# Performance work log

Hardware: AMD Instinct MI355X
Metric: run time of the kernel (lower is better)

The kernel has to match this reference:

```python
import jax, jax.numpy as jnp
import numpy as np

N = 131072        # total packed tokens
D = 256           # input_dim
E = 512           # embed_dim
B = 16            # number of batches (len(cu_seqlens)-1)
NLAYERS = 64      # max distinct layer ids per batch


def setup_inputs() -> dict:
    key = jax.random.key(0)
    ks = jax.random.split(key, 8)
    feats = jax.random.normal(ks[0], (N, D), dtype=jnp.float32)
    cu_seqlens = jnp.arange(0, N + 1, N // B, dtype=jnp.int32)  # [B+1]
    layer_ids = jax.random.randint(ks[1], (N,), 0, NLAYERS, dtype=jnp.int32)
    # Linear params stored as [in, out] (y = x @ W + b), matching torch Linear math.
    Wa = jax.random.normal(ks[2], (D, 1), jnp.float32) * 0.05
    ba = jnp.zeros((1,), jnp.float32)
    W1 = jax.random.normal(ks[3], (3 * D, E), jnp.float32) * 0.02
    b1 = jnp.zeros((E,), jnp.float32)
    W2 = jax.random.normal(ks[4], (E, D), jnp.float32) * 0.02
    b2 = jnp.zeros((D,), jnp.float32)
    Wc = jax.random.normal(ks[5], (2 * D, D), jnp.float32) * 0.02
    bc = jnp.zeros((D,), jnp.float32)
    return dict(feats=feats, cu_seqlens=cu_seqlens, layer_ids=layer_ids,
                Wa=Wa, ba=ba, W1=W1, b1=b1, W2=W2, b2=b2, Wc=Wc, bc=bc)


def _forward(feats, cu_seqlens, layer_ids, Wa, ba, W1, b1, W2, b2, Wc, bc):
    n = feats.shape[0]
    nseg = B * NLAYERS
    # batch id of each token from the cumulative sequence lengths
    batch_ids = jnp.searchsorted(cu_seqlens, jnp.arange(n, dtype=jnp.int32), side='right') - 1
    # global (batch, layer) segment id -> vectorizes the per-batch scatter loop
    seg = batch_ids * NLAYERS + layer_ids

    counts = jax.ops.segment_sum(jnp.ones((n,), feats.dtype), seg, num_segments=nseg)  # [nseg]
    sums = jax.ops.segment_sum(feats, seg, num_segments=nseg)                           # [nseg, D]
    avg_pool = sums / jnp.maximum(counts, 1.0)[:, None]
    max_pool = jax.ops.segment_max(feats, seg, num_segments=nseg)
    max_pool = jnp.where(counts[:, None] > 0, max_pool, 0.0)  # empty segments -> 0 (never gathered)

    # attention softmax over all tokens of each batch (dim=0 within the batch slice)
    logits = (feats @ Wa + ba)[:, 0]                                    # [n]
    m = jax.ops.segment_max(logits, batch_ids, num_segments=B)          # [B]
    e = jnp.exp(logits - m[batch_ids])
    z = jax.ops.segment_sum(e, batch_ids, num_segments=B)               # [B]
    w = e / z[batch_ids]                                                # [n]
    attention_pool = jax.ops.segment_sum(feats * w[:, None], seg, num_segments=nseg)

    pooled = jnp.concatenate([avg_pool, max_pool, attention_pool], axis=1)  # [nseg, 3D]
    h = jax.nn.gelu(pooled @ W1 + b1, approximate=False)
    layer_feats = h @ W2 + b2                                               # [nseg, D]

    gathered = layer_feats[seg]                                             # [n, D]
    out = jnp.concatenate([gathered, feats], axis=1) @ Wc + bc              # [n, D]
    return out


def reference(feats, cu_seqlens, layer_ids, Wa, ba, W1, b1, W2, b2, Wc, bc):
    return _forward(feats, cu_seqlens, layer_ids, Wa, ba, W1, b1, W2, b2, Wc, bc)
```

## Files before the change

kernel.cpp:

```cpp
#include <hip/hip_runtime.h>
#include <hip/hip_bf16.h>
#include <math.h>

#define NTOK 131072
#define DIM  256
#define EDIM 512
#define NB   16
#define NL   64
#define NSEG (NB*NL)
#define K3D  768
#define K2D  512
#define HB   64
#define K4CH 256

typedef __attribute__((ext_vector_type(8))) short short8;
typedef __attribute__((ext_vector_type(4))) float f32x4;

static __device__ __forceinline__ unsigned fcode(float x){
  unsigned b = __float_as_uint(x);
  return (b & 0x80000000u) ? ~b : (b | 0x80000000u);
}
static __device__ __forceinline__ float fdecode(unsigned c){
  unsigned b = (c & 0x80000000u) ? (c ^ 0x80000000u) : ~c;
  return __uint_as_float(b);
}
#define NEG_INF_CODE 0x007FFFFFu

static __device__ __forceinline__ short f2bf(float x){
  union { __hip_bfloat16 h; short s; } u; u.h = __float2bfloat16(x); return u.s;
}
static __device__ __forceinline__ float bf2f(short s){
  union { float f; unsigned u; } u; u.u = ((unsigned)(unsigned short)s) << 16; return u.f;
}

__global__ __launch_bounds__(256) void k0_transpose(const float* __restrict__ W1, const float* __restrict__ W2,
                                                    const float* __restrict__ Wc,
                                                    short* __restrict__ W1t, short* __restrict__ W2t,
                                                    short* __restrict__ Wct, unsigned* __restrict__ bmax){
  if (blockIdx.x == 0 && threadIdx.x < NB) bmax[threadIdx.x] = NEG_INF_CODE;
  __shared__ short tile[64][65];
  int b = blockIdx.x;
  const float* src; short* dst; int K, N, kt, nt;
  if (b < 96){ src=W1; dst=W1t; K=768; N=512; kt=b/8;  nt=b%8;  }
  else if (b < 128){ int c=b-96;  src=W2; dst=W2t; K=512; N=256; kt=c/4; nt=c%4; }
  else             { int c=b-128; src=Wc; dst=Wct; K=512; N=256; kt=c/4; nt=c%4; }
  int k0 = kt*64, n0 = nt*64;
  for (int e = threadIdx.x; e < 4096; e += 256){
    int r = e >> 6, c = e & 63;
    tile[c][r] = f2bf(src[(size_t)(k0+r)*N + n0 + c]);
  }
  __syncthreads();
  for (int e = threadIdx.x; e < 4096; e += 256){
    int r = e >> 6, c = e & 63;
    dst[(size_t)(n0+r)*K + k0 + c] = tile[r][c];
  }
}

template<int WRITEB>
__global__ __launch_bounds__(256) void k1_logits(const float* __restrict__ feats, const int* __restrict__ cu,
    const int* __restrict__ layer_ids, const float* __restrict__ Wa, const float* __restrict__ ba,
    float* __restrict__ logits, int* __restrict__ seg, unsigned* __restrict__ bmax,
    short* __restrict__ featsb){
  __shared__ int      lcu[NB];
  __shared__ unsigned lbm[NB];
  int tid = threadIdx.x;
  if (tid < NB){ lcu[tid] = cu[tid+1]; lbm[tid] = NEG_INF_CODE; }
  int s = tid & 15;
  int rowoff = tid >> 4;
  float4 w0 = *(const float4*)(Wa + s*4);
  float4 w1 = *(const float4*)(Wa + 64 + s*4);
  float4 w2 = *(const float4*)(Wa + 128 + s*4);
  float4 w3 = *(const float4*)(Wa + 192 + s*4);
  float bav = ba[0];
  __syncthreads();
#pragma unroll
  for (int it = 0; it < 4; ++it){
    int r = (blockIdx.x + it*2048)*16 + rowoff;
    const float4* fp = (const float4*)(feats + (size_t)r*DIM);
    float4 x0 = fp[s], x1 = fp[16+s], x2 = fp[32+s], x3 = fp[48+s];
    float a = x0.x*w0.x + x0.y*w0.y + x0.z*w0.z + x0.w*w0.w
            + x1.x*w1.x + x1.y*w1.y + x1.z*w1.z + x1.w*w1.w
            + x2.x*w2.x + x2.y*w2.y + x2.z*w2.z + x2.w*w2.w
            + x3.x*w3.x + x3.y*w3.y + x3.z*w3.z + x3.w*w3.w;
    if (WRITEB){
      short4* ob = (short4*)(featsb + (size_t)r*DIM);
      short4 v;
      v.x=f2bf(x0.x); v.y=f2bf(x0.y); v.z=f2bf(x0.z); v.w=f2bf(x0.w); ob[s]    = v;
      v.x=f2bf(x1.x); v.y=f2bf(x1.y); v.z=f2bf(x1.z); v.w=f2bf(x1.w); ob[16+s] = v;
      v.x=f2bf(x2.x); v.y=f2bf(x2.y); v.z=f2bf(x2.z); v.w=f2bf(x2.w); ob[32+s] = v;
      v.x=f2bf(x3.x); v.y=f2bf(x3.y); v.z=f2bf(x3.z); v.w=f2bf(x3.w); ob[48+s] = v;
    }
    a += __shfl_xor(a, 1);
    a += __shfl_xor(a, 2);
    a += __shfl_xor(a, 4);
    a += __shfl_xor(a, 8);
    if (s == 0){
      float lg = a + bav;
      logits[r] = lg;
      int b = 0;
#pragma unroll
      for (int j = 0; j < NB-1; ++j) b += (lcu[j] <= r) ? 1 : 0;
      seg[r] = b*NL + layer_ids[r];
      atomicMax(&lbm[b], fcode(lg));
    }
  }
  __syncthreads();
  if (tid < NB && lbm[tid] != NEG_INF_CODE) atomicMax(&bmax[tid], lbm[tid]);
}

__global__ __launch_bounds__(256) void k2_softmax_z(const float* __restrict__ logits, const int* __restrict__ cu,
    const unsigned* __restrict__ bmax, float* __restrict__ bz){
  __shared__ float red[256];
  int b = blockIdx.x;
  int s = cu[b], e = cu[b+1];
  float m = fdecode(bmax[b]);
  float acc = 0.f;
  for (int i = s + threadIdx.x; i < e; i += 256)
    acc += expf(logits[i] - m);
  red[threadIdx.x] = acc; __syncthreads();
  for (int off = 128; off; off >>= 1){
    if (threadIdx.x < off) red[threadIdx.x] += red[threadIdx.x + off];
    __syncthreads();
  }
  if (threadIdx.x == 0) bz[b] = red[0];
}

__global__ __launch_bounds__(256) void k3a_hist(const int* __restrict__ seg, int* __restrict__ hist){
  __shared__ int h[NSEG];
  for (int i = threadIdx.x; i < NSEG; i += 256) h[i] = 0;
  __syncthreads();
  int base = blockIdx.x * (NTOK/HB);
  for (int i = threadIdx.x; i < NTOK/HB; i += 256) atomicAdd(&h[seg[base+i]], 1);
  __syncthreads();
  for (int i = threadIdx.x; i < NSEG; i += 256) hist[(size_t)blockIdx.x*NSEG + i] = h[i];
}

__global__ __launch_bounds__(1024) void k3b_scan(int* __restrict__ hist, int* __restrict__ segstart){
  __shared__ int sc[NSEG];
  int s = threadIdx.x;
  int tot = 0;
#pragma unroll
  for (int b = 0; b < HB; ++b) tot += hist[(size_t)b*NSEG + s];
  sc[s] = tot; __syncthreads();
  for (int off = 1; off < NSEG; off <<= 1){
    int v = (s >= off) ? sc[s-off] : 0;
    __syncthreads();
    sc[s] += v;
    __syncthreads();
  }
  int segbase = sc[s] - tot;
  segstart[s] = segbase;
  if (s == 0) segstart[NSEG] = NTOK;
  int run = segbase;
#pragma unroll
  for (int b = 0; b < HB; ++b){
    int c = hist[(size_t)b*NSEG + s];
    hist[(size_t)b*NSEG + s] = run;
    run += c;
  }
}

__global__ __launch_bounds__(256) void k3c_scatter(const int* __restrict__ seg, const int* __restrict__ hist,
                                                   int* __restrict__ sorted){
  __shared__ int cur[NSEG];
  for (int i = threadIdx.x; i < NSEG; i += 256) cur[i] = hist[(size_t)blockIdx.x*NSEG + i];
  __syncthreads();
  int base = blockIdx.x * (NTOK/HB);
  for (int i = threadIdx.x; i < NTOK/HB; i += 256){
    int sg = seg[base+i];
    int p = atomicAdd(&cur[sg], 1);
    sorted[p] = base+i;
  }
}

template<int USEB>
__global__ __launch_bounds__(256) void k4_pool(const float* __restrict__ feats, const short* __restrict__ featsb,
    const int* __restrict__ sorted, const int* __restrict__ segstart,
    const float* __restrict__ logits, const unsigned* __restrict__ bmax, const float* __restrict__ bz,
    short* __restrict__ pooledb){
  __shared__ float redS[4][DIM];
  __shared__ float redM[4][DIM];
  __shared__ float redA[4][DIM];
  __shared__ int   ltok[K4CH];
  __shared__ float lwgt[K4CH];
  int sgi = blockIdx.x;
  int b = sgi >> 6;
  int s = segstart[sgi], e = segstart[sgi+1];
  int cnt = e - s;
  float m = fdecode(bmax[b]);
  float invz = 1.0f / bz[b];
  int lane = threadIdx.x & 63, grp = threadIdx.x >> 6;
  float4 sum = make_float4(0.f,0.f,0.f,0.f), att = make_float4(0.f,0.f,0.f,0.f);
  float4 mx  = make_float4(-INFINITY,-INFINITY,-INFINITY,-INFINITY);
  for (int c0 = s; c0 < e; c0 += K4CH){
    int csz = min(K4CH, e - c0);
    for (int j = threadIdx.x; j < csz; j += 256){
      int t = sorted[c0 + j];
      ltok[j] = t;
      lwgt[j] = expf(logits[t] - m) * invz;
    }
    __syncthreads();
    for (int j = grp; j < csz; j += 4){
      int tok = ltok[j];
      float w = lwgt[j];
      float4 x;
      if (USEB){
        short4 h = *(const short4*)(featsb + (size_t)tok*DIM + lane*4);
        x = make_float4(bf2f(h.x), bf2f(h.y), bf2f(h.z), bf2f(h.w));
      } else {
        x = *(const float4*)(feats + (size_t)tok*DIM + lane*4);
      }
      sum.x += x.x; sum.y += x.y; sum.z += x.z; sum.w += x.w;
      mx.x = fmaxf(mx.x, x.x); mx.y = fmaxf(mx.y, x.y);
      mx.z = fmaxf(mx.z, x.z); mx.w = fmaxf(mx.w, x.w);
      att.x += x.x*w; att.y += x.y*w; att.z += x.z*w; att.w += x.w*w;
    }
    __syncthreads();
  }
  *(float4*)&redS[grp][lane*4] = sum;
  *(float4*)&redM[grp][lane*4] = mx;
  *(float4*)&redA[grp][lane*4] = att;
  __syncthreads();
  int d = threadIdx.x;
  float rs = redS[0][d] + redS[1][d] + redS[2][d] + redS[3][d];
  float rm = fmaxf(fmaxf(redM[0][d], redM[1][d]), fmaxf(redM[2][d], redM[3][d]));
  float ra = redA[0][d] + redA[1][d] + redA[2][d] + redA[3][d];
  float inv = 1.0f / (float)(cnt > 1 ? cnt : 1);
  size_t rb_ = (size_t)sgi * K3D;
  pooledb[rb_ + d]         = f2bf(rs * inv);
  pooledb[rb_ + DIM + d]   = f2bf(cnt > 0 ? rm : 0.f);
  pooledb[rb_ + 2*DIM + d] = f2bf(ra);
}

template<int GELU>
__global__ __launch_bounds__(256) void gemm64(const short* __restrict__ A, const short* __restrict__ Bt,
    const float* __restrict__ bias, short* __restrict__ Cout, int K, int ldc){
  __shared__ short lA[64][40];
  __shared__ short lB[64][40];
  int tid = threadIdx.x;
  int wave = tid >> 6, lane = tid & 63;
  int wm = wave >> 1, wn = wave & 1;
  int rb = blockIdx.x * 64, cb = blockIdx.y * 64;
  int l15 = lane & 15, lg = lane >> 4;
  f32x4 acc[2][2] = {};
  int srow = tid >> 2, skg = tid & 3;
  for (int ks = 0; ks < K; ks += 32){
    __syncthreads();
    *(short8*)&lA[srow][skg*8] = *(const short8*)(A  + (size_t)(rb+srow)*K + ks + skg*8);
    *(short8*)&lB[srow][skg*8] = *(const short8*)(Bt + (size_t)(cb+srow)*K + ks + skg*8);
    __syncthreads();
    short8 af[2], bf[2];
#pragma unroll
    for (int f = 0; f < 2; ++f){
      af[f] = *(const short8*)&lA[wm*32 + f*16 + l15][lg*8];
      bf[f] = *(const short8*)&lB[wn*32 + f*16 + l15][lg*8];
    }
#pragma unroll
    for (int fm = 0; fm < 2; ++fm)
#pragma unroll
      for (int fn = 0; fn < 2; ++fn)
        acc[fm][fn] = __builtin_amdgcn_mfma_f32_16x16x32_bf16(af[fm], bf[fn], acc[fm][fn], 0, 0, 0);
  }
#pragma unroll
  for (int fm = 0; fm < 2; ++fm)
#pragma unroll
    for (int fn = 0; fn < 2; ++fn){
      int col = cb + wn*32 + fn*16 + l15;
      float bcv = bias[col];
#pragma unroll
      for (int r = 0; r < 4; ++r){
        int row = rb + wm*32 + fm*16 + lg*4 + r;
        float v = acc[fm][fn][r] + bcv;
        if (GELU) v = 0.5f * v * (1.0f + erff(v * 0.70710678118f));
        Cout[(size_t)row*ldc + col] = f2bf(v);
      }
    }
}

template<int USEB>
__global__ __launch_bounds__(1024, 4) void k5_final(const float* __restrict__ feats,
    const short* __restrict__ featsb, const short* __restrict__ lfb,
    const int* __restrict__ seg, const short* __restrict__ Wct, const float* __restrict__ bc,
    float* __restrict__ out){
  __shared__ short lA[2][128][72];
  __shared__ short lB[2][256][72];
  int tid = threadIdx.x;
  int wave = tid >> 6, lane = tid & 63;
  int wm = wave >> 2, wn = wave & 3;
  int bid = (int)blockIdx.x;
  int swz = (bid & 7) * 128 + (bid >> 3);
  int rb = swz * 128;
  int l15 = lane & 15, lg = lane >> 4;
  int arow = tid >> 3, akg = tid & 7;
  int brow0 = tid >> 3, brow1 = (tid + 1024) >> 3, bkg = tid & 7;
  const short* lfbp = lfb + (size_t)seg[rb + arow]*DIM + akg*8;
  const short* fbp  = featsb + (size_t)(rb + arow)*DIM + akg*8;
  const float* ffp  = feats  + (size_t)(rb + arow)*DIM + akg*8;
  const short* wp0 = Wct + (size_t)brow0*K2D + bkg*8;
  const short* wp1 = Wct + (size_t)brow1*K2D + bkg*8;
  short8 ra, rb0, rb1; float4 fa0, fa1;
  auto LOAD = [&](int t){
    if (t < 4)      ra = *(const short8*)(lfbp + t*64);
    else if (USEB)  ra = *(const short8*)(fbp + (t-4)*64);
    else { const float* p = ffp + (size_t)(t-4)*64; fa0 = *(const float4*)p; fa1 = *(const float4*)(p+4); }
    rb0 = *(const short8*)(wp0 + t*64);
    rb1 = *(const short8*)(wp1 + t*64);
  };
  auto WRITE = [&](int t){
    int buf = t & 1;
    if (!USEB && t >= 4){
      short8 v;
      v[0]=f2bf(fa0.x); v[1]=f2bf(fa0.y); v[2]=f2bf(fa0.z); v[3]=f2bf(fa0.w);
      v[4]=f2bf(fa1.x); v[5]=f2bf(fa1.y); v[6]=f2bf(fa1.z); v[7]=f2bf(fa1.w);
      *(short8*)&lA[buf][arow][akg*8] = v;
    } else {
      *(short8*)&lA[buf][arow][akg*8] = ra;
    }
    *(short8*)&lB[buf][brow0][bkg*8] = rb0;
    *(short8*)&lB[buf][brow1][bkg*8] = rb1;
  };
  f32x4 acc[2][4] = {};
  LOAD(0); WRITE(0); LOAD(1);
  __syncthreads();
  for (int ks = 0; ks < 8; ++ks){
    int cur = ks & 1;
    if (ks < 7) WRITE(ks+1);
    if (ks < 6) LOAD(ks+2);
#pragma unroll
    for (int kk = 0; kk < 2; ++kk){
      short8 af[2], bf[4];
#pragma unroll
      for (int f = 0; f < 2; ++f)
        af[f] = *(const short8*)&lA[cur][wm*32 + f*16 + l15][kk*32 + lg*8];
#pragma unroll
      for (int f = 0; f < 4; ++f)
        bf[f] = *(const short8*)&lB[cur][wn*64 + f*16 + l15][kk*32 + lg*8];
#pragma unroll
      for (int fm = 0; fm < 2; ++fm)
#pragma unroll
        for (int fn = 0; fn < 4; ++fn)
          acc[fm][fn] = __builtin_amdgcn_mfma_f32_16x16x32_bf16(af[fm], bf[fn], acc[fm][fn], 0, 0, 0);
    }
    __syncthreads();
  }
#pragma unroll
  for (int fm = 0; fm < 2; ++fm)
#pragma unroll
    for (int fn = 0; fn < 4; ++fn){
      int col = wn*64 + fn*16 + l15;
      float bcv = bc[col];
#pragma unroll
      for (int r = 0; r < 4; ++r){
        int row = rb + wm*32 + fm*16 + lg*4 + r;
        out[(size_t)row*DIM + col] = acc[fm][fn][r] + bcv;
      }
    }
}

extern "C" void kernel_launch(void* const* d_in, const int* in_sizes, int n_in,
                              void* d_out, int out_size, void* d_ws, size_t ws_size,
                              hipStream_t stream){
  const float* feats     = (const float*)d_in[0];
  const int*   cu        = (const int*)d_in[1];
  const int*   layer_ids = (const int*)d_in[2];
  const float* Wa        = (const float*)d_in[3];
  const float* ba        = (const float*)d_in[4];
  const float* W1        = (const float*)d_in[5];
  const float* b1        = (const float*)d_in[6];
  const float* W2        = (const float*)d_in[7];
  const float* b2        = (const float*)d_in[8];
  const float* Wc        = (const float*)d_in[9];
  const float* bc        = (const float*)d_in[10];
  float* out = (float*)d_out;

  char* w = (char*)d_ws;
  auto alloc = [&](size_t bytes)->char*{ char* p = w; w += (bytes + 255) & ~255ull; return p; };
  float*    logits  = (float*)   alloc((size_t)NTOK*4);
  int*      seg     = (int*)     alloc((size_t)NTOK*4);
  int*      sorted  = (int*)     alloc((size_t)NTOK*4);
  int*      hist    = (int*)     alloc((size_t)NSEG*HB*4);
  int*      segstart= (int*)     alloc((size_t)(NSEG+1)*4);
  unsigned* bmax    = (unsigned*)alloc(NB*4);
  float*    bz      = (float*)   alloc(NB*4);
  short*    W1t     = (short*)   alloc((size_t)512*768*2);
  short*    W2t     = (short*)   alloc((size_t)256*512*2);
  short*    Wct     = (short*)   alloc((size_t)256*512*2);
  short*    pooledb = (short*)   alloc((size_t)NSEG*K3D*2);
  short*    hb      = (short*)   alloc((size_t)NSEG*EDIM*2);
  short*    lfb     = (short*)   alloc((size_t)NSEG*DIM*2);
  short*    featsb  = (short*)   alloc((size_t)NTOK*DIM*2);
  size_t need = (size_t)(w - (char*)d_ws);
  bool useb = (ws_size >= need);

  k0_transpose<<<dim3(160), dim3(256), 0, stream>>>(W1, W2, Wc, W1t, W2t, Wct, bmax);
  if (useb)
    k1_logits<1><<<dim3(2048), dim3(256), 0, stream>>>(feats, cu, layer_ids, Wa, ba, logits, seg, bmax, featsb);
  else
    k1_logits<0><<<dim3(2048), dim3(256), 0, stream>>>(feats, cu, layer_ids, Wa, ba, logits, seg, bmax, featsb);
  k2_softmax_z<<<dim3(16), dim3(256), 0, stream>>>(logits, cu, bmax, bz);
  k3a_hist<<<dim3(HB), dim3(256), 0, stream>>>(seg, hist);
  k3b_scan<<<dim3(1), dim3(1024), 0, stream>>>(hist, segstart);
  k3c_scatter<<<dim3(HB), dim3(256), 0, stream>>>(seg, hist, sorted);
  if (useb)
    k4_pool<1><<<dim3(NSEG), dim3(256), 0, stream>>>(feats, featsb, sorted, segstart, logits, bmax, bz, pooledb);
  else
    k4_pool<0><<<dim3(NSEG), dim3(256), 0, stream>>>(feats, featsb, sorted, segstart, logits, bmax, bz, pooledb);
  gemm64<1><<<dim3(16, 8), dim3(256), 0, stream>>>(pooledb, W1t, b1, hb, 768, 512);
  gemm64<0><<<dim3(16, 4), dim3(256), 0, stream>>>(hb, W2t, b2, lfb, 512, 256);
  if (useb)
    k5_final<1><<<dim3(1024), dim3(1024), 0, stream>>>(feats, featsb, lfb, seg, Wct, bc, out);
  else
    k5_final<0><<<dim3(1024), dim3(1024), 0, stream>>>(feats, featsb, lfb, seg, Wct, bc, out);
}
```

Before: 186.1 us.

## Merge histogram and softmax-normalizer kernels; retile final GEMM to 128x128 blocks

Combines the softmax denominator kernel and the segment histogram kernel into one launch, with extra blocks taking the per-batch z reduction, to drop one launch. The final output GEMM changes from 1024-thread blocks covering 128 rows by all 256 columns to 512-thread blocks covering a 128x128 tile, with twice as many blocks and each wave computing 64x32. This halves shared memory per block and should improve occupancy and scheduling. The cost is that the A operand (gathered layer features and feats) is loaded twice, once per column half.

```diff
diff --git a/kernel.cpp b/kernel.cpp
--- a/kernel.cpp
+++ b/kernel.cpp
@@ -108,31 +108,33 @@
   if (tid < NB && lbm[tid] != NEG_INF_CODE) atomicMax(&bmax[tid], lbm[tid]);
 }
 
-__global__ __launch_bounds__(256) void k2_softmax_z(const float* __restrict__ logits, const int* __restrict__ cu,
+__global__ __launch_bounds__(256) void k23_hist_z(const int* __restrict__ seg, int* __restrict__ hist,
+    const float* __restrict__ logits, const int* __restrict__ cu,
     const unsigned* __restrict__ bmax, float* __restrict__ bz){
-  __shared__ float red[256];
-  int b = blockIdx.x;
-  int s = cu[b], e = cu[b+1];
-  float m = fdecode(bmax[b]);
-  float acc = 0.f;
-  for (int i = s + threadIdx.x; i < e; i += 256)
-    acc += expf(logits[i] - m);
-  red[threadIdx.x] = acc; __syncthreads();
-  for (int off = 128; off; off >>= 1){
-    if (threadIdx.x < off) red[threadIdx.x] += red[threadIdx.x + off];
-    __syncthreads();
-  }
-  if (threadIdx.x == 0) bz[b] = red[0];
-}
-
-__global__ __launch_bounds__(256) void k3a_hist(const int* __restrict__ seg, int* __restrict__ hist){
   __shared__ int h[NSEG];
-  for (int i = threadIdx.x; i < NSEG; i += 256) h[i] = 0;
-  __syncthreads();
-  int base = blockIdx.x * (NTOK/HB);
-  for (int i = threadIdx.x; i < NTOK/HB; i += 256) atomicAdd(&h[seg[base+i]], 1);
-  __syncthreads();
-  for (int i = threadIdx.x; i < NSEG; i += 256) hist[(size_t)blockIdx.x*NSEG + i] = h[i];
+  int bid = blockIdx.x;
+  if (bid < HB){
+    for (int i = threadIdx.x; i < NSEG; i += 256) h[i] = 0;
+    __syncthreads();
+    int base = bid * (NTOK/HB);
+    for (int i = threadIdx.x; i < NTOK/HB; i += 256) atomicAdd(&h[seg[base+i]], 1);
+    __syncthreads();
+    for (int i = threadIdx.x; i < NSEG; i += 256) hist[(size_t)bid*NSEG + i] = h[i];
+  } else {
+    float* red = (float*)h;
+    int b = bid - HB;
+    int s = cu[b], e = cu[b+1];
+    float m = fdecode(bmax[b]);
+    float acc = 0.f;
+    for (int i = s + threadIdx.x; i < e; i += 256)
+      acc += expf(logits[i] - m);
+    red[threadIdx.x] = acc; __syncthreads();
+    for (int off = 128; off; off >>= 1){
+      if (threadIdx.x < off) red[threadIdx.x] += red[threadIdx.x + off];
+      __syncthreads();
+    }
+    if (threadIdx.x == 0) bz[b] = red[0];
+  }
 }
 
 __global__ __launch_bounds__(1024) void k3b_scan(int* __restrict__ hist, int* __restrict__ segstart){
@@ -278,31 +280,41 @@
 }
 
 template<int USEB>
-__global__ __launch_bounds__(1024, 4) void k5_final(const float* __restrict__ feats,
+__global__ __launch_bounds__(512, 4) void k5_final(const float* __restrict__ feats,
     const short* __restrict__ featsb, const short* __restrict__ lfb,
     const int* __restrict__ seg, const short* __restrict__ Wct, const float* __restrict__ bc,
     float* __restrict__ out){
   __shared__ short lA[2][128][72];
-  __shared__ short lB[2][256][72];
+  __shared__ short lB[2][128][72];
   int tid = threadIdx.x;
   int wave = tid >> 6, lane = tid & 63;
   int wm = wave >> 2, wn = wave & 3;
   int bid = (int)blockIdx.x;
-  int swz = (bid & 7) * 128 + (bid >> 3);
-  int rb = swz * 128;
+  int swz = (bid & 7) * 256 + (bid >> 3);
+  int rb = (swz >> 1) * 128;
+  int cb = (swz & 1) * 128;
   int l15 = lane & 15, lg = lane >> 4;
-  int arow = tid >> 3, akg = tid & 7;
-  int brow0 = tid >> 3, brow1 = (tid + 1024) >> 3, bkg = tid & 7;
-  const short* lfbp = lfb + (size_t)seg[rb + arow]*DIM + akg*8;
-  const short* fbp  = featsb + (size_t)(rb + arow)*DIM + akg*8;
-  const float* ffp  = feats  + (size_t)(rb + arow)*DIM + akg*8;
-  const short* wp0 = Wct + (size_t)brow0*K2D + bkg*8;
-  const short* wp1 = Wct + (size_t)brow1*K2D + bkg*8;
-  short8 ra, rb0, rb1; float4 fa0, fa1;
+  int arow0 = tid >> 3, arow1 = (tid >> 3) + 64, akg = tid & 7;
+  const short* lfbp0 = lfb + (size_t)seg[rb + arow0]*DIM + akg*8;
+  const short* lfbp1 = lfb + (size_t)seg[rb + arow1]*DIM + akg*8;
+  const short* fbp0  = featsb + (size_t)(rb + arow0)*DIM + akg*8;
+  const short* fbp1  = featsb + (size_t)(rb + arow1)*DIM + akg*8;
+  const float* ffp0  = feats  + (size_t)(rb + arow0)*DIM + akg*8;
+  const float* ffp1  = feats  + (size_t)(rb + arow1)*DIM + akg*8;
+  const short* wp0 = Wct + (size_t)(cb + arow0)*K2D + akg*8;
+  const short* wp1 = Wct + (size_t)(cb + arow1)*K2D + akg*8;
+  short8 ra0, ra1, rb0, rb1; float4 fa00, fa01, fa10, fa11;
   auto LOAD = [&](int t){
-    if (t < 4)      ra = *(const short8*)(lfbp + t*64);
-    else if (USEB)  ra = *(const short8*)(fbp + (t-4)*64);
-    else { const float* p = ffp + (size_t)(t-4)*64; fa0 = *(const float4*)p; fa1 = *(const float4*)(p+4); }
+    if (t < 4){
+      ra0 = *(const short8*)(lfbp0 + t*64);
+      ra1 = *(const short8*)(lfbp1 + t*64);
+    } else if (USEB){
+      ra0 = *(const short8*)(fbp0 + (t-4)*64);
+      ra1 = *(const short8*)(fbp1 + (t-4)*64);
+    } else {
+      const float* p0 = ffp0 + (size_t)(t-4)*64; fa00 = *(const float4*)p0; fa01 = *(const float4*)(p0+4);
+      const float* p1 = ffp1 + (size_t)(t-4)*64; fa10 = *(const float4*)p1; fa11 = *(const float4*)(p1+4);
+    }
     rb0 = *(const short8*)(wp0 + t*64);
     rb1 = *(const short8*)(wp1 + t*64);
   };
@@ -310,16 +322,20 @@
     int buf = t & 1;
     if (!USEB && t >= 4){
       short8 v;
-      v[0]=f2bf(fa0.x); v[1]=f2bf(fa0.y); v[2]=f2bf(fa0.z); v[3]=f2bf(fa0.w);
-      v[4]=f2bf(fa1.x); v[5]=f2bf(fa1.y); v[6]=f2bf(fa1.z); v[7]=f2bf(fa1.w);
-      *(short8*)&lA[buf][arow][akg*8] = v;
+      v[0]=f2bf(fa00.x); v[1]=f2bf(fa00.y); v[2]=f2bf(fa00.z); v[3]=f2bf(fa00.w);
+      v[4]=f2bf(fa01.x); v[5]=f2bf(fa01.y); v[6]=f2bf(fa01.z); v[7]=f2bf(fa01.w);
+      *(short8*)&lA[buf][arow0][akg*8] = v;
+      v[0]=f2bf(fa10.x); v[1]=f2bf(fa10.y); v[2]=f2bf(fa10.z); v[3]=f2bf(fa10.w);
+      v[4]=f2bf(fa11.x); v[5]=f2bf(fa11.y); v[6]=f2bf(fa11.z); v[7]=f2bf(fa11.w);
+      *(short8*)&lA[buf][arow1][akg*8] = v;
     } else {
-      *(short8*)&lA[buf][arow][akg*8] = ra;
-    }
-    *(short8*)&lB[buf][brow0][bkg*8] = rb0;
-    *(short8*)&lB[buf][brow1][bkg*8] = rb1;
+      *(short8*)&lA[buf][arow0][akg*8] = ra0;
+      *(short8*)&lA[buf][arow1][akg*8] = ra1;
+    }
+    *(short8*)&lB[buf][arow0][akg*8] = rb0;
+    *(short8*)&lB[buf][arow1][akg*8] = rb1;
   };
-  f32x4 acc[2][4] = {};
+  f32x4 acc[4][2] = {};
   LOAD(0); WRITE(0); LOAD(1);
   __syncthreads();
   for (int ks = 0; ks < 8; ++ks){
@@ -328,30 +344,30 @@
     if (ks < 6) LOAD(ks+2);
 #pragma unroll
     for (int kk = 0; kk < 2; ++kk){
-      short8 af[2], bf[4];
+      short8 af[4], bf[2];
+#pragma unroll
+      for (int f = 0; f < 4; ++f)
+        af[f] = *(const short8*)&lA[cur][wm*64 + f*16 + l15][kk*32 + lg*8];
 #pragma unroll
       for (int f = 0; f < 2; ++f)
-        af[f] = *(const short8*)&lA[cur][wm*32 + f*16 + l15][kk*32 + lg*8];
-#pragma unroll
-      for (int f = 0; f < 4; ++f)
-        bf[f] = *(const short8*)&lB[cur][wn*64 + f*16 + l15][kk*32 + lg*8];
-#pragma unroll
-      for (int fm = 0; fm < 2; ++fm)
-#pragma unroll
-        for (int fn = 0; fn < 4; ++fn)
+        bf[f] = *(const short8*)&lB[cur][wn*32 + f*16 + l15][kk*32 + lg*8];
+#pragma unroll
+      for (int fm = 0; fm < 4; ++fm)
+#pragma unroll
+        for (int fn = 0; fn < 2; ++fn)
           acc[fm][fn] = __builtin_amdgcn_mfma_f32_16x16x32_bf16(af[fm], bf[fn], acc[fm][fn], 0, 0, 0);
     }
     __syncthreads();
   }
 #pragma unroll
-  for (int fm = 0; fm < 2; ++fm)
-#pragma unroll
-    for (int fn = 0; fn < 4; ++fn){
-      int col = wn*64 + fn*16 + l15;
+  for (int fm = 0; fm < 4; ++fm)
+#pragma unroll
+    for (int fn = 0; fn < 2; ++fn){
+      int col = cb + wn*32 + fn*16 + l15;
       float bcv = bc[col];
 #pragma unroll
       for (int r = 0; r < 4; ++r){
-        int row = rb + wm*32 + fm*16 + lg*4 + r;
+        int row = rb + wm*64 + fm*16 + lg*4 + r;
         out[(size_t)row*DIM + col] = acc[fm][fn][r] + bcv;
       }
     }
@@ -397,8 +413,7 @@
     k1_logits<1><<<dim3(2048), dim3(256), 0, stream>>>(feats, cu, layer_ids, Wa, ba, logits, seg, bmax, featsb);
   else
     k1_logits<0><<<dim3(2048), dim3(256), 0, stream>>>(feats, cu, layer_ids, Wa, ba, logits, seg, bmax, featsb);
-  k2_softmax_z<<<dim3(16), dim3(256), 0, stream>>>(logits, cu, bmax, bz);
-  k3a_hist<<<dim3(HB), dim3(256), 0, stream>>>(seg, hist);
+  k23_hist_z<<<dim3(HB + NB), dim3(256), 0, stream>>>(seg, hist, logits, cu, bmax, bz);
   k3b_scan<<<dim3(1), dim3(1024), 0, stream>>>(hist, segstart);
   k3c_scatter<<<dim3(HB), dim3(256), 0, stream>>>(seg, hist, sorted);
   if (useb)
@@ -408,7 +423,7 @@
   gemm64<1><<<dim3(16, 8), dim3(256), 0, stream>>>(pooledb, W1t, b1, hb, 768, 512);
   gemm64<0><<<dim3(16, 4), dim3(256), 0, stream>>>(hb, W2t, b2, lfb, 512, 256);
   if (useb)
-    k5_final<1><<<dim3(1024), dim3(1024), 0, stream>>>(feats, featsb, lfb, seg, Wct, bc, out);
+    k5_final<1><<<dim3(2048), dim3(512), 0, stream>>>(feats, featsb, lfb, seg, Wct, bc, out);
   else
-    k5_final<0><<<dim3(1024), dim3(1024), 0, stream>>>(feats, featsb, lfb, seg, Wct, bc, out);
-}
+    k5_final<0><<<dim3(2048), dim3(512), 0, stream>>>(feats, featsb, lfb, seg, Wct, bc, out);
+}
```

Result: faster. 178.1 us (-4.3%).
